# Kernel tuning notes

Hardware: AMD Instinct MI355X
Metric: run time of the kernel (lower is better)

The kernel has to match this reference:

```python
import jax, jax.numpy as jnp
import numpy as np

D_MODEL, D_FF, D_H = 1024, 4096, 64
D_H2 = D_H // 2


def layer_norm(x, w, b, eps=1e-5):
    mu = x.mean(-1, keepdims=True)
    var = x.var(-1, keepdims=True)
    return (x - mu) / jnp.sqrt(var + eps) * w + b


def gelu(x):
    return jax.nn.gelu(x, approximate=False)


def setup_inputs() -> dict:
    key = jax.random.key(0)
    ks = jax.random.split(key, 12)
    s = 0.02
    return {
        "x": jax.random.normal(ks[0], (4, 1024, D_MODEL), jnp.float32),
        "W1": jax.random.normal(ks[1], (D_FF, D_MODEL), jnp.float32) * s,
        "W2": jax.random.normal(ks[2], (D_MODEL, D_FF), jnp.float32) * s,
        "Wr1": jax.random.normal(ks[3], (D_MODEL, D_MODEL), jnp.float32) * s,
        "Wr2": jax.random.normal(ks[4], (D_FF, D_MODEL), jnp.float32) * s,
        "ln_w": jnp.ones((D_MODEL,), jnp.float32),
        "ln_b": jnp.zeros((D_MODEL,), jnp.float32),
        "phi1_w": jax.random.normal(ks[5], (D_H2, 1), jnp.float32) * s,
        "phi1_b": jnp.zeros((D_H2,), jnp.float32),
        "phi_ln1_w": jnp.ones((D_H2,), jnp.float32),
        "phi_ln1_b": jnp.zeros((D_H2,), jnp.float32),
        "phi2_w": jax.random.normal(ks[6], (D_H, D_H2), jnp.float32) * s,
        "phi2_b": jnp.zeros((D_H,), jnp.float32),
        "phi_ln2_w": jnp.ones((D_H,), jnp.float32),
        "phi_ln2_b": jnp.zeros((D_H,), jnp.float32),
        "rho1_w": jax.random.normal(ks[7], (D_H * 2, D_H), jnp.float32) * s,
        "rho1_b": jnp.zeros((D_H * 2,), jnp.float32),
        "rho2_w": jax.random.normal(ks[8], (1, D_H * 2), jnp.float32) * s,
        "rho2_b": jnp.zeros((1,), jnp.float32),
        "top_k": 256,
    }


def reference(x, W1, W2, Wr1, Wr2, ln_w, ln_b,
              phi1_w, phi1_b, phi_ln1_w, phi_ln1_b,
              phi2_w, phi2_b, phi_ln2_w, phi_ln2_b,
              rho1_w, rho1_b, rho2_w, rho2_b, top_k):
    batch, seq, d_model = x.shape
    x_flat = x.reshape(-1, d_model)                      # [T, D]
    T = x_flat.shape[0]

    # Router scores (2-layer MLP router)
    x_norm = layer_norm(x_flat, ln_w, ln_b)
    h = gelu(x_norm @ Wr1.T)
    scores = h @ Wr2.T                                   # [T, d_ff]
    top_idx = jax.lax.top_k(scores, top_k)[1]            # [T, K]

    # Dense GEMM + data-dependent top-k mask + GELU
    z = x_flat @ W1.T                                    # [T, d_ff]
    rows = jnp.arange(T)[:, None]
    mask = jnp.zeros_like(z).at[rows, top_idx].set(1.0)
    a = gelu(z * mask)

    # DeepSets manifold mixing on the selected activations
    a_sel = jnp.take_along_axis(a, top_idx, axis=-1)     # [T, K]
    e = a_sel[..., None] * phi1_w[:, 0] + phi1_b         # Linear(1 -> D_H2): [T, K, D_H2]
    e = gelu(layer_norm(e, phi_ln1_w, phi_ln1_b))
    e = layer_norm(e @ phi2_w.T + phi2_b, phi_ln2_w, phi_ln2_b)  # [T, K, D_H]
    ctx = e.mean(axis=1, keepdims=True)                  # permutation-invariant aggregate
    c = e + ctx
    r = gelu(c @ rho1_w.T + rho1_b)                      # [T, K, 2*D_H] (Dropout -> identity)
    man = (r @ rho2_w.T + rho2_b)[..., 0]                # [T, K]

    # Scatter manifold outputs back into the d_ff lane layout
    a_man = jnp.zeros_like(a).at[rows, top_idx].set(man)
    out = a_man @ W2.T                                   # [T, D]
    return out.reshape(batch, seq, d_model)
```

## Files before the change

kernel.cpp:

```cpp
#include <hip/hip_runtime.h>

#define T_TOKENS 4096
#define DM 1024
#define DF 4096
#define KSEL 256
#define DH 64
#define DH2 32
#define BAND_DELTA 1.0e-2f
#define CAP_ROW 256

typedef __attribute__((ext_vector_type(8))) short short8;
typedef __attribute__((ext_vector_type(4))) float f32x4;
typedef __attribute__((ext_vector_type(2))) float f32x2;

__device__ __forceinline__ f32x2 pkfma(f32x2 a, f32x2 b, f32x2 c) {
    return __builtin_elementwise_fma(a, b, c);
}

__device__ __forceinline__ float gelu_f(float x) {
    return 0.5f * x * (1.0f + erff(x * 0.70710678118654752440f));
}

__device__ __forceinline__ float erf_fast(float x) {
    float ax = __builtin_fabsf(x);
    float t = __builtin_amdgcn_rcpf(fmaf(0.3275911f, ax, 1.0f));
    float p = 1.061405429f;
    p = fmaf(p, t, -1.453152027f);
    p = fmaf(p, t, 1.421413741f);
    p = fmaf(p, t, -0.284496736f);
    p = fmaf(p, t, 0.254829592f);
    float e = __builtin_amdgcn_exp2f(-ax * ax * 1.44269504088896f);
    float r = fmaf(-p * t, e, 1.0f);
    return __builtin_copysignf(r, x);
}
__device__ __forceinline__ float gelu_fast(float x) {
    return 0.5f * x * (1.0f + erf_fast(x * 0.70710678118654752440f));
}

__device__ __forceinline__ unsigned short bf16_rne(float f) {
    unsigned u = __float_as_uint(f);
    unsigned r = (u + 0x7FFFu + ((u >> 16) & 1u)) >> 16;
    return (unsigned short)r;
}
__device__ __forceinline__ float bf16_to_f(unsigned short h) {
    return __uint_as_float(((unsigned)h) << 16);
}

__global__ __launch_bounds__(256) void ln_kernel(const float* __restrict__ x,
                                                 const float* __restrict__ w,
                                                 const float* __restrict__ b,
                                                 float* __restrict__ out) {
    int row = blockIdx.x;
    int tid = threadIdx.x;
    const float4 v = ((const float4*)(x + (size_t)row * DM))[tid];
    float s = v.x + v.y + v.z + v.w;
    float s2 = v.x * v.x + v.y * v.y + v.z * v.z + v.w * v.w;
#pragma unroll
    for (int off = 32; off > 0; off >>= 1) {
        s += __shfl_xor(s, off);
        s2 += __shfl_xor(s2, off);
    }
    __shared__ float ss[4], ss2[4];
    int wave = tid >> 6;
    if ((tid & 63) == 0) { ss[wave] = s; ss2[wave] = s2; }
    __syncthreads();
    s = ss[0] + ss[1] + ss[2] + ss[3];
    s2 = ss2[0] + ss2[1] + ss2[2] + ss2[3];
    float mu = s * (1.0f / DM);
    float var = s2 * (1.0f / DM) - mu * mu;
    float rs = rsqrtf(var + 1e-5f);
    const float4 wv = ((const float4*)w)[tid];
    const float4 bv = ((const float4*)b)[tid];
    float4 o;
    o.x = (v.x - mu) * rs * wv.x + bv.x;
    o.y = (v.y - mu) * rs * wv.y + bv.y;
    o.z = (v.z - mu) * rs * wv.z + bv.z;
    o.w = (v.w - mu) * rs * wv.w + bv.w;
    ((float4*)(out + (size_t)row * DM))[tid] = o;
}

__global__ __launch_bounds__(256) void gemm_f32_128(const float* __restrict__ A,
                                                    const float* __restrict__ B,
                                                    float* __restrict__ C,
                                                    int M, int N, int K, int fuse_gelu) {
    __shared__ __align__(16) float As[16][132];
    __shared__ __align__(16) float Bs[16][132];
    int tid = threadIdx.x;
    int bm = blockIdx.y * 128, bn = blockIdx.x * 128;
    int tr = tid >> 4, tc = tid & 15;

    float4 avr[2], bvr[2];
    auto g_load = [&](int k0) {
#pragma unroll
        for (int s = 0; s < 2; s++) {
            int i = tid * 2 + s;
            int r = i >> 2, q = i & 3;
            avr[s] = *(const float4*)(A + (size_t)(bm + r) * K + k0 + q * 4);
            bvr[s] = *(const float4*)(B + (size_t)(bn + r) * K + k0 + q * 4);
        }
    };

    float acc[8][8] = {};
    g_load(0);
    for (int k0 = 0; k0 < K; k0 += 16) {
        __syncthreads();
#pragma unroll
        for (int s = 0; s < 2; s++) {
            int i = tid * 2 + s;
            int r = i >> 2, q = i & 3;
            As[q * 4 + 0][r] = avr[s].x; As[q * 4 + 1][r] = avr[s].y;
            As[q * 4 + 2][r] = avr[s].z; As[q * 4 + 3][r] = avr[s].w;
            Bs[q * 4 + 0][r] = bvr[s].x; Bs[q * 4 + 1][r] = bvr[s].y;
            Bs[q * 4 + 2][r] = bvr[s].z; Bs[q * 4 + 3][r] = bvr[s].w;
        }
        __syncthreads();
        if (k0 + 16 < K) g_load(k0 + 16);
#pragma unroll
        for (int kk = 0; kk < 16; kk++) {
            float4 a0 = *(const float4*)&As[kk][tr * 4];
            float4 a1 = *(const float4*)&As[kk][64 + tr * 4];
            float4 b0 = *(const float4*)&Bs[kk][tc * 4];
            float4 b1 = *(const float4*)&Bs[kk][64 + tc * 4];
            float ar[8] = {a0.x, a0.y, a0.z, a0.w, a1.x, a1.y, a1.z, a1.w};
            float br[8] = {b0.x, b0.y, b0.z, b0.w, b1.x, b1.y, b1.z, b1.w};
#pragma unroll
            for (int i = 0; i < 8; i++)
#pragma unroll
                for (int j = 0; j < 8; j++)
                    acc[i][j] = fmaf(ar[i], br[j], acc[i][j]);
        }
    }
#pragma unroll
    for (int i = 0; i < 8; i++) {
        int row = bm + (i < 4 ? tr * 4 + i : 64 + tr * 4 + (i - 4));
        float* cp = C + (size_t)row * N + bn;
        float4 o0, o1;
        if (fuse_gelu) {
            o0 = make_float4(gelu_f(acc[i][0]), gelu_f(acc[i][1]), gelu_f(acc[i][2]), gelu_f(acc[i][3]));
            o1 = make_float4(gelu_f(acc[i][4]), gelu_f(acc[i][5]), gelu_f(acc[i][6]), gelu_f(acc[i][7]));
        } else {
            o0 = make_float4(acc[i][0], acc[i][1], acc[i][2], acc[i][3]);
            o1 = make_float4(acc[i][4], acc[i][5], acc[i][6], acc[i][7]);
        }
        *(float4*)(cp + tc * 4) = o0;
        *(float4*)(cp + 64 + tc * 4) = o1;
    }
}

__global__ __launch_bounds__(256) void gemm_bf16(const short* __restrict__ A,
                                                 const short* __restrict__ B,
                                                 float* __restrict__ C,
                                                 int M, int N, int K,
                                                 int lda, int ldb, int beta) {
    __shared__ __align__(16) short As[128 * 64];
    __shared__ __align__(16) short Bs[128 * 64];
    int tid = threadIdx.x;
    int bm = blockIdx.y * 128, bn = blockIdx.x * 128;
    int lane = tid & 63, wave = tid >> 6;
    int wm = (wave >> 1) * 64, wn = (wave & 1) * 64;
    int quad = lane >> 4, l16 = lane & 15;
    int sr = tid >> 3, scp = tid & 7;

    short8 areg[4], breg[4];
    auto g_load = [&](int k0) {
#pragma unroll
        for (int j = 0; j < 4; j++) {
            int r = j * 32 + sr;
            int cl = scp ^ (r & 7);
            areg[j] = *(const short8*)(A + (size_t)(bm + r) * lda + k0 + cl * 8);
            breg[j] = *(const short8*)(B + (size_t)(bn + r) * ldb + k0 + cl * 8);
        }
    };

    f32x4 acc[4][4] = {};
    g_load(0);
    for (int k0 = 0; k0 < K; k0 += 64) {
        __syncthreads();
#pragma unroll
        for (int j = 0; j < 4; j++) {
            *(short8*)(As + (j * 256 + tid) * 8) = areg[j];
            *(short8*)(Bs + (j * 256 + tid) * 8) = breg[j];
        }
        __syncthreads();
        if (k0 + 64 < K) g_load(k0 + 64);
#pragma unroll
        for (int kk = 0; kk < 2; kk++) {
            short8 af[4], bf[4];
#pragma unroll
            for (int tm = 0; tm < 4; tm++) {
                int m = wm + tm * 16 + l16;
                int cp = (kk * 4 + quad) ^ (m & 7);
                af[tm] = *(const short8*)(As + m * 64 + cp * 8);
            }
#pragma unroll
            for (int tn = 0; tn < 4; tn++) {
                int n = wn + tn * 16 + l16;
                int cp = (kk * 4 + quad) ^ (n & 7);
                bf[tn] = *(const short8*)(Bs + n * 64 + cp * 8);
            }
#pragma unroll
            for (int tm = 0; tm < 4; tm++)
#pragma unroll
                for (int tn = 0; tn < 4; tn++)
                    acc[tm][tn] = __builtin_amdgcn_mfma_f32_16x16x32_bf16(
                        af[tm], bf[tn], acc[tm][tn], 0, 0, 0);
        }
    }
#pragma unroll
    for (int tm = 0; tm < 4; tm++)
#pragma unroll
        for (int tn = 0; tn < 4; tn++) {
            int row0 = bm + wm + tm * 16 + quad * 4;
            int col = bn + wn + tn * 16 + l16;
#pragma unroll
            for (int r = 0; r < 4; r++) {
                float* p = C + (size_t)(row0 + r) * N + col;
                float v = acc[tm][tn][r];
                if (beta) v += *p;
                *p = v;
            }
        }
}

__global__ __launch_bounds__(256) void cvt_split_cat_kernel(const float* __restrict__ x,
                                                            short* __restrict__ cat,
                                                            int n4, int lo_first) {
    int i = blockIdx.x * 256 + threadIdx.x;
    if (i >= n4) return;
    float4 v = ((const float4*)x)[i];
    ushort4 h, l;
    h.x = bf16_rne(v.x); l.x = bf16_rne(v.x - bf16_to_f(h.x));
    h.y = bf16_rne(v.y); l.y = bf16_rne(v.y - bf16_to_f(h.y));
    h.z = bf16_rne(v.z); l.z = bf16_rne(v.z - bf16_to_f(h.z));
    h.w = bf16_rne(v.w); l.w = bf16_rne(v.w - bf16_to_f(h.w));
    int row = i >> 8;
    int col4 = i & 255;
    size_t base = (size_t)row * (2 * DM);
    size_t off_a = base + col4 * 4;
    size_t off_b = base + DM + col4 * 4;
    ((ushort4*)(cat + (lo_first ? off_b : off_a)))[0] = h;
    ((ushort4*)(cat + (lo_first ? off_a : off_b)))[0] = l;
}

__global__ __launch_bounds__(256) void cvt_bf16_kernel(const float* __restrict__ x,
                                                       short* __restrict__ y, int n4) {
    int i = blockIdx.x * 256 + threadIdx.x;
    if (i >= n4) return;
    float4 v = ((const float4*)x)[i];
    ushort4 h;
    h.x = bf16_rne(v.x); h.y = bf16_rne(v.y);
    h.z = bf16_rne(v.z); h.w = bf16_rne(v.w);
    ((ushort4*)y)[i] = h;
}

__device__ __forceinline__ unsigned sortable(float f) {
    unsigned u = __float_as_uint(f);
    return (u & 0x80000000u) ? ~u : (u | 0x80000000u);
}
__device__ __forceinline__ float unsortable(unsigned k) {
    unsigned b = (k & 0x80000000u) ? (k & 0x7FFFFFFFu) : ~k;
    return __uint_as_float(b);
}

__global__ __launch_bounds__(256) void topk_band_kernel(const float* __restrict__ scores,
                                                        int* __restrict__ cand,
                                                        int* __restrict__ cnt) {
    int row = blockIdx.x;
    int tid = threadIdx.x;
    __shared__ unsigned s_keys[DF];
    __shared__ int hist[256];
    __shared__ int sufs[256];
    __shared__ int s_misc[4];
    __shared__ int s_cnt;

    const float* sr = scores + (size_t)row * DF;
    for (int i = tid; i < DF; i += 256) s_keys[i] = sortable(sr[i]);
    if (tid == 0) s_cnt = 0;

    unsigned prefix = 0;
    int krem = KSEL;
    for (int pass = 0; pass < 4; pass++) {
        int shift = 24 - pass * 8;
        unsigned hmask = (pass == 0) ? 0u : (0xFFFFFFFFu << (shift + 8));
        hist[tid] = 0;
        __syncthreads();
        for (int i = tid; i < DF; i += 256) {
            unsigned u = s_keys[i];
            if ((u & hmask) == prefix) atomicAdd(&hist[(u >> shift) & 0xFF], 1);
        }
        __syncthreads();
        sufs[tid] = hist[tid];
        __syncthreads();
#pragma unroll
        for (int off = 1; off < 256; off <<= 1) {
            int add = (tid + off < 256) ? sufs[tid + off] : 0;
            __syncthreads();
            sufs[tid] += add;
            __syncthreads();
        }
        if (sufs[tid] >= krem && (tid == 255 || sufs[tid + 1] < krem)) {
            s_misc[0] = tid;
            s_misc[1] = sufs[tid] - hist[tid];
        }
        __syncthreads();
        prefix |= ((unsigned)s_misc[0]) << shift;
        krem -= s_misc[1];
        __syncthreads();
    }
    float vf = unsortable(prefix);
    for (int i = tid; i < DF; i += 256) {
        float d = sr[i] - vf;
        if (__builtin_fabsf(d) <= BAND_DELTA) {
            int p = atomicAdd(&s_cnt, 1);
            if (p < CAP_ROW) cand[(size_t)row * CAP_ROW + p] = i;
        }
    }
    __syncthreads();
    if (tid == 0) cnt[row] = s_cnt < CAP_ROW ? s_cnt : CAP_ROW;
}

__global__ __launch_bounds__(256) void rescore_kernel(const float* __restrict__ h,
                                                      const float* __restrict__ Wr2,
                                                      const int* __restrict__ cand,
                                                      const int* __restrict__ cnt,
                                                      float* __restrict__ scores) {
    int row = blockIdx.x;
    int lane = threadIdx.x & 63;
    int wv = threadIdx.x >> 6;
    int n = cnt[row];
    const float4* hp = (const float4*)(h + (size_t)row * DM);
    for (int c = wv; c < n; c += 4) {
        int col = cand[(size_t)row * CAP_ROW + c];
        const float4* wp = (const float4*)(Wr2 + (size_t)col * DM);
        float s = 0.f;
#pragma unroll
        for (int j = 0; j < 4; j++) {
            float4 a = hp[lane + 64 * j];
            float4 b = wp[lane + 64 * j];
            s = fmaf(a.x, b.x, s);
            s = fmaf(a.y, b.y, s);
            s = fmaf(a.z, b.z, s);
            s = fmaf(a.w, b.w, s);
        }
#pragma unroll
        for (int st = 1; st < 64; st <<= 1) s += __shfl_xor(s, st);
        if (lane == 0) scores[(size_t)row * DF + col] = s;
    }
}

__global__ __launch_bounds__(256) void topk_kernel(const float* __restrict__ scores,
                                                   int* __restrict__ top_idx) {
    int row = blockIdx.x;
    int tid = threadIdx.x;
    __shared__ unsigned s_keys[DF];
    __shared__ int hist[256];
    __shared__ int sufs[256];
    __shared__ int s_misc[4];
    __shared__ int s_wsums[4];

    const float* sr = scores + (size_t)row * DF;
    for (int i = tid; i < DF; i += 256) s_keys[i] = sortable(sr[i]);

    unsigned prefix = 0;
    int krem = KSEL;
    for (int pass = 0; pass < 4; pass++) {
        int shift = 24 - pass * 8;
        unsigned hmask = (pass == 0) ? 0u : (0xFFFFFFFFu << (shift + 8));
        hist[tid] = 0;
        __syncthreads();
        for (int i = tid; i < DF; i += 256) {
            unsigned u = s_keys[i];
            if ((u & hmask) == prefix) atomicAdd(&hist[(u >> shift) & 0xFF], 1);
        }
        __syncthreads();
        sufs[tid] = hist[tid];
        __syncthreads();
#pragma unroll
        for (int off = 1; off < 256; off <<= 1) {
            int add = (tid + off < 256) ? sufs[tid + off] : 0;
            __syncthreads();
            sufs[tid] += add;
            __syncthreads();
        }
        if (sufs[tid] >= krem && (tid == 255 || sufs[tid + 1] < krem)) {
            s_misc[0] = tid;
            s_misc[1] = sufs[tid] - hist[tid];
        }
        __syncthreads();
        prefix |= ((unsigned)s_misc[0]) << shift;
        krem -= s_misc[1];
        __syncthreads();
    }
    unsigned v = prefix;
    if (tid == 0) s_misc[2] = 0;
    __syncthreads();
    int* out = top_idx + (size_t)row * KSEL;
    for (int i = tid; i < DF; i += 256) {
        if (s_keys[i] > v) {
            int p = atomicAdd(&s_misc[2], 1);
            out[p] = i;
        }
    }
    __syncthreads();
    int base = s_misc[2];
    int lane = tid & 63, wave = tid >> 6;
    int taken = 0;
    for (int chunk = 0; chunk < DF / 256; chunk++) {
        int i = chunk * 256 + tid;
        int flag = (s_keys[i] == v) ? 1 : 0;
        unsigned long long mb = __ballot(flag);
        int before = __popcll(mb & ((1ULL << lane) - 1ULL));
        if (lane == 0) s_wsums[wave] = __popcll(mb);
        __syncthreads();
        int woff = 0;
#pragma unroll
        for (int w = 0; w < 4; w++) if (w < wave) woff += s_wsums[w];
        int total = s_wsums[0] + s_wsums[1] + s_wsums[2] + s_wsums[3];
        int excl = woff + before;
        if (flag && (taken + excl) < krem) out[base + taken + excl] = i;
        taken += total;
        __syncthreads();
    }
}

__global__ __launch_bounds__(256) void manifold_kernel(
    const float* __restrict__ z, const int* __restrict__ top_idx,
    const float* __restrict__ phi1_w, const float* __restrict__ phi1_b,
    const float* __restrict__ ln1w, const float* __restrict__ ln1b,
    const float* __restrict__ phi2_w, const float* __restrict__ phi2_b,
    const float* __restrict__ ln2w, const float* __restrict__ ln2b,
    const short* __restrict__ rho1b16, const float* __restrict__ rho1_b,
    const float* __restrict__ rho2_w, const float* __restrict__ rho2_b,
    float* __restrict__ man) {
    __shared__ __align__(16) short c_lds[256 * DH];
    __shared__ __align__(16) short w_lds[128 * DH];
    __shared__ float s_ctxp[4 * DH];
    __shared__ float s_ctx[DH];
    __shared__ float s_rho1b[2 * DH];
    __shared__ float s_rho2w[2 * DH];

    int tid = threadIdx.x;
    int t = blockIdx.x;
    int lane = tid & 63, wave = tid >> 6;
    int l16 = lane & 15, quad = lane >> 4;

    for (int b = tid; b < 128 * 8; b += 256) {
        int row = b >> 3, j = b & 7;
        *(short8*)(w_lds + row * DH + ((j ^ (row & 7)) * 8)) =
            *(const short8*)(rho1b16 + row * DH + j * 8);
    }
    if (tid < 2 * DH) { s_rho1b[tid] = rho1_b[tid]; s_rho2w[tid] = rho2_w[tid]; }

    int idx = top_idx[(size_t)t * KSEL + tid];
    float a = gelu_fast(z[(size_t)t * DF + idx]);
    f32x2 a2 = {a, a};

    f32x2 gv[DH2 / 2];
    f32x2 sv = {0.f, 0.f}, qv = {0.f, 0.f};
#pragma unroll
    for (int i = 0; i < DH2 / 2; i++) {
        f32x2 w = ((const f32x2*)phi1_w)[i];
        f32x2 b = ((const f32x2*)phi1_b)[i];
        f32x2 e = pkfma(a2, w, b);
        gv[i] = e;
        sv = sv + e;
        qv = pkfma(e, e, qv);
    }
    float s = sv.x + sv.y, s2 = qv.x + qv.y;
    float mu = s * (1.0f / DH2);
    float rs = rsqrtf(s2 * (1.0f / DH2) - mu * mu + 1e-5f);
    f32x2 muv = {mu, mu}, rsv = {rs, rs};
#pragma unroll
    for (int i = 0; i < DH2 / 2; i++) {
        f32x2 t2 = (gv[i] - muv) * rsv;
        t2 = pkfma(t2, ((const f32x2*)ln1w)[i], ((const f32x2*)ln1b)[i]);
        gv[i] = (f32x2){gelu_fast(t2.x), gelu_fast(t2.y)};
    }

    f32x2 hv[DH / 2];
#pragma unroll
    for (int j2 = 0; j2 < DH / 2; j2++) {
        const f32x2* wa = (const f32x2*)(phi2_w + (2 * j2) * DH2);
        const f32x2* wb = (const f32x2*)(phi2_w + (2 * j2 + 1) * DH2);
        f32x2 ra = {phi2_b[2 * j2], 0.f};
        f32x2 rb = {phi2_b[2 * j2 + 1], 0.f};
#pragma unroll
        for (int i = 0; i < DH2 / 2; i++) {
            ra = pkfma(gv[i], wa[i], ra);
            rb = pkfma(gv[i], wb[i], rb);
        }
        hv[j2] = (f32x2){ra.x + ra.y, rb.x + rb.y};
    }

    f32x2 tsv = {0.f, 0.f}, tqv = {0.f, 0.f};
#pragma unroll
    for (int j2 = 0; j2 < DH / 2; j2++) {
        tsv = tsv + hv[j2];
        tqv = pkfma(hv[j2], hv[j2], tqv);
    }
    float tsum = tsv.x + tsv.y, tsq = tqv.x + tqv.y;
    float mu2 = tsum * (1.0f / DH);
    float rs2 = rsqrtf(tsq * (1.0f / DH) - mu2 * mu2 + 1e-5f);
    f32x2 mu2v = {mu2, mu2}, rs2v = {rs2, rs2};
#pragma unroll
    for (int j2 = 0; j2 < DH / 2; j2++) {
        f32x2 t2 = (hv[j2] - mu2v) * rs2v;
        hv[j2] = pkfma(t2, ((const f32x2*)ln2w)[j2], ((const f32x2*)ln2b)[j2]);
    }

#pragma unroll
    for (int j2 = 0; j2 < DH / 2; j2++) {
        float vx = hv[j2].x, vy = hv[j2].y;
#pragma unroll
        for (int st = 1; st < 64; st <<= 1) {
            vx += __shfl_xor(vx, st);
            vy += __shfl_xor(vy, st);
        }
        if (lane == 0) {
            s_ctxp[wave * DH + 2 * j2] = vx;
            s_ctxp[wave * DH + 2 * j2 + 1] = vy;
        }
    }
    __syncthreads();
    if (tid < DH)
        s_ctx[tid] = (s_ctxp[tid] + s_ctxp[DH + tid] + s_ctxp[2 * DH + tid] +
                      s_ctxp[3 * DH + tid]) * (1.0f / KSEL);
    __syncthreads();

#pragma unroll
    for (int j = 0; j < 8; j++) {
        short8 pk;
#pragma unroll
        for (int i2 = 0; i2 < 4; i2++) {
            f32x2 v = hv[4 * j + i2] + ((const f32x2*)s_ctx)[4 * j + i2];
            pk[2 * i2] = (short)bf16_rne(v.x);
            pk[2 * i2 + 1] = (short)bf16_rne(v.y);
        }
        *(short8*)(c_lds + tid * DH + ((j ^ (tid & 7)) * 8)) = pk;
    }
    __syncthreads();

    int wbase = wave * 64;
    short8 af[4][2];
#pragma unroll
    for (int tm = 0; tm < 4; tm++)
#pragma unroll
        for (int kf = 0; kf < 2; kf++) {
            int m = wbase + tm * 16 + l16;
            int cl = (kf * 4 + quad) ^ (m & 7);
            af[tm][kf] = *(const short8*)(c_lds + m * DH + cl * 8);
        }
    float mpart[4][4] = {};
#pragma unroll
    for (int tn = 0; tn < 8; tn++) {
        int n = tn * 16 + l16;
        short8 bf[2];
#pragma unroll
        for (int kf = 0; kf < 2; kf++) {
            int cl = (kf * 4 + quad) ^ (n & 7);
            bf[kf] = *(const short8*)(w_lds + n * DH + cl * 8);
        }
        f32x4 acc[4] = {};
#pragma unroll
        for (int kf = 0; kf < 2; kf++)
#pragma unroll
            for (int tm = 0; tm < 4; tm++)
                acc[tm] = __builtin_amdgcn_mfma_f32_16x16x32_bf16(
                    af[tm][kf], bf[kf], acc[tm], 0, 0, 0);
        float b1 = s_rho1b[n];
        float w2v = s_rho2w[n];
#pragma unroll
        for (int tm = 0; tm < 4; tm++)
#pragma unroll
            for (int r = 0; r < 4; r++)
                mpart[tm][r] = fmaf(gelu_fast(acc[tm][r] + b1), w2v, mpart[tm][r]);
    }
#pragma unroll
    for (int tm = 0; tm < 4; tm++)
#pragma unroll
        for (int r = 0; r < 4; r++) {
            float v = mpart[tm][r];
            v += __shfl_xor(v, 1);
            v += __shfl_xor(v, 2);
            v += __shfl_xor(v, 4);
            v += __shfl_xor(v, 8);
            mpart[tm][r] = v;
        }
    if (l16 == 0) {
        float b2 = rho2_b[0];
#pragma unroll
        for (int tm = 0; tm < 4; tm++)
#pragma unroll
            for (int r = 0; r < 4; r++)
                man[(size_t)t * KSEL + wbase + tm * 16 + quad * 4 + r] =
                    mpart[tm][r] + b2;
    }
}

__global__ __launch_bounds__(256) void scatter_bf16_kernel(const float* __restrict__ man,
                                                           const int* __restrict__ top_idx,
                                                           short* __restrict__ a_man) {
    int t = blockIdx.x, k = threadIdx.x;
    a_man[(size_t)t * DF + top_idx[(size_t)t * KSEL + k]] =
        (short)bf16_rne(man[(size_t)t * KSEL + k]);
}

extern "C" void kernel_launch(void* const* d_in, const int* in_sizes, int n_in,
                              void* d_out, int out_size, void* d_ws, size_t ws_size,
                              hipStream_t stream) {
    const float* x      = (const float*)d_in[0];
    const float* W1     = (const float*)d_in[1];
    const float* W2     = (const float*)d_in[2];
    const float* Wr1    = (const float*)d_in[3];
    const float* Wr2    = (const float*)d_in[4];
    const float* ln_w   = (const float*)d_in[5];
    const float* ln_b   = (const float*)d_in[6];
    const float* phi1_w = (const float*)d_in[7];
    const float* phi1_b = (const float*)d_in[8];
    const float* pl1w   = (const float*)d_in[9];
    const float* pl1b   = (const float*)d_in[10];
    const float* phi2_w = (const float*)d_in[11];
    const float* phi2_b = (const float*)d_in[12];
    const float* pl2w   = (const float*)d_in[13];
    const float* pl2b   = (const float*)d_in[14];
    const float* rho1_w = (const float*)d_in[15];
    const float* rho1_b = (const float*)d_in[16];
    const float* rho2_w = (const float*)d_in[17];
    const float* rho2_b = (const float*)d_in[18];
    float* out = (float*)d_out;

    char* ws = (char*)d_ws;
    size_t off = 0;
    auto alloc = [&](size_t bytes) {
        char* p = ws + off;
        off += (bytes + 255) & ~(size_t)255;
        return p;
    };
    float* xn     = (float*)alloc(sizeof(float) * (size_t)T_TOKENS * DM);
    float* h      = (float*)alloc(sizeof(float) * (size_t)T_TOKENS * DM);
    float* scores = (float*)alloc(sizeof(float) * (size_t)T_TOKENS * DF);
    float* z      = (float*)alloc(sizeof(float) * (size_t)T_TOKENS * DF);
    int*   tidx   = (int*)alloc(sizeof(int) * (size_t)T_TOKENS * KSEL);
    float* man    = (float*)alloc(sizeof(float) * (size_t)T_TOKENS * KSEL);
    int*   cand   = (int*)alloc(sizeof(int) * (size_t)T_TOKENS * CAP_ROW);
    int*   cnt    = (int*)alloc(sizeof(int) * (size_t)T_TOKENS);
    short* rho1b16 = (short*)alloc(sizeof(short) * 2 * DH * DH);

    short* h_hi   = (short*)z;
    short* wr2_hi = (short*)z + (size_t)T_TOKENS * DM;
    short* xcat  = (short*)xn;
    short* w1cat = (short*)h;
    short* amanb = (short*)scores;
    short* w2b   = (short*)z;

    ln_kernel<<<T_TOKENS, 256, 0, stream>>>(x, ln_w, ln_b, xn);
    gemm_f32_128<<<dim3(DM / 128, T_TOKENS / 128), 256, 0, stream>>>(xn, Wr1, h, T_TOKENS, DM, DM, 1);
    cvt_bf16_kernel<<<(T_TOKENS * DM / 4 + 255) / 256, 256, 0, stream>>>(h, h_hi, T_TOKENS * DM / 4);
    cvt_bf16_kernel<<<(DF * DM / 4 + 255) / 256, 256, 0, stream>>>(Wr2, wr2_hi, DF * DM / 4);
    gemm_bf16<<<dim3(DF / 128, T_TOKENS / 128), 256, 0, stream>>>(
        h_hi, wr2_hi, scores, T_TOKENS, DF, DM, DM, DM, 0);
    topk_band_kernel<<<T_TOKENS, 256, 0, stream>>>(scores, cand, cnt);
    rescore_kernel<<<T_TOKENS, 256, 0, stream>>>(h, Wr2, cand, cnt, scores);
    topk_kernel<<<T_TOKENS, 256, 0, stream>>>(scores, tidx);
    cvt_split_cat_kernel<<<(T_TOKENS * DM / 4 + 255) / 256, 256, 0, stream>>>(x, xcat, T_TOKENS * DM / 4, 0);
    cvt_split_cat_kernel<<<(DF * DM / 4 + 255) / 256, 256, 0, stream>>>(W1, w1cat, DF * DM / 4, 1);
    cvt_bf16_kernel<<<(2 * DH * DH / 4 + 255) / 256, 256, 0, stream>>>(rho1_w, rho1b16, 2 * DH * DH / 4);
    gemm_bf16<<<dim3(DF / 128, T_TOKENS / 128), 256, 0, stream>>>(
        xcat, w1cat + DM, z, T_TOKENS, DF, DM, 2 * DM, 2 * DM, 0);
    gemm_bf16<<<dim3(DF / 128, T_TOKENS / 128), 256, 0, stream>>>(
        xcat, w1cat, z, T_TOKENS, DF, 2 * DM, 2 * DM, 2 * DM, 1);
    manifold_kernel<<<T_TOKENS, 256, 0, stream>>>(z, tidx, phi1_w, phi1_b, pl1w, pl1b,
                                                  phi2_w, phi2_b, pl2w, pl2b,
                                                  rho1b16, rho1_b, rho2_w, rho2_b, man);
    hipMemsetAsync(amanb, 0, sizeof(short) * (size_t)T_TOKENS * DF, stream);
    scatter_bf16_kernel<<<T_TOKENS, 256, 0, stream>>>(man, tidx, amanb);
    cvt_bf16_kernel<<<(DM * DF / 4 + 255) / 256, 256, 0, stream>>>(W2, w2b, DM * DF / 4);
    gemm_bf16<<<dim3(DM / 128, T_TOKENS / 128), 256, 0, stream>>>(
        amanb, w2b, out, T_TOKENS, DM, DF, DF, DF, 0);
}
```

Baseline: 929.4 us.

## Use single fp16 GEMM for W1/W2 and replace full top-k with band-only selection

Replaces the split hi/lo bf16 W1 GEMM (two passes, effective K of 2048 plus 1024) with a single fp16 GEMM on a new f16 MFMA kernel, and switches the W2 GEMM to fp16 as well. The top-k path no longer rescans all 4096 scores a second time. The band kernel writes confidently-above indices directly, and a small rank-based selection over the rescored band candidates fills the remaining slots. This cuts GEMM work and one full radix pass per row, at the cost of fp16 range and precision risk for the z values that feed top-k activations.

```diff
diff --git a/kernel.cpp b/kernel.cpp
--- a/kernel.cpp
+++ b/kernel.cpp
@@ -10,6 +10,7 @@
 #define CAP_ROW 256
 
 typedef __attribute__((ext_vector_type(8))) short short8;
+typedef __attribute__((ext_vector_type(8))) _Float16 half8;
 typedef __attribute__((ext_vector_type(4))) float f32x4;
 typedef __attribute__((ext_vector_type(2))) float f32x2;
 
@@ -41,9 +42,6 @@
     unsigned u = __float_as_uint(f);
     unsigned r = (u + 0x7FFFu + ((u >> 16) & 1u)) >> 16;
     return (unsigned short)r;
-}
-__device__ __forceinline__ float bf16_to_f(unsigned short h) {
-    return __uint_as_float(((unsigned)h) << 16);
 }
 
 __global__ __launch_bounds__(256) void ln_kernel(const float* __restrict__ x,
@@ -222,24 +220,76 @@
         }
 }
 
-__global__ __launch_bounds__(256) void cvt_split_cat_kernel(const float* __restrict__ x,
-                                                            short* __restrict__ cat,
-                                                            int n4, int lo_first) {
-    int i = blockIdx.x * 256 + threadIdx.x;
-    if (i >= n4) return;
-    float4 v = ((const float4*)x)[i];
-    ushort4 h, l;
-    h.x = bf16_rne(v.x); l.x = bf16_rne(v.x - bf16_to_f(h.x));
-    h.y = bf16_rne(v.y); l.y = bf16_rne(v.y - bf16_to_f(h.y));
-    h.z = bf16_rne(v.z); l.z = bf16_rne(v.z - bf16_to_f(h.z));
-    h.w = bf16_rne(v.w); l.w = bf16_rne(v.w - bf16_to_f(h.w));
-    int row = i >> 8;
-    int col4 = i & 255;
-    size_t base = (size_t)row * (2 * DM);
-    size_t off_a = base + col4 * 4;
-    size_t off_b = base + DM + col4 * 4;
-    ((ushort4*)(cat + (lo_first ? off_b : off_a)))[0] = h;
-    ((ushort4*)(cat + (lo_first ? off_a : off_b)))[0] = l;
+__global__ __launch_bounds__(256) void gemm_f16(const short* __restrict__ A,
+                                                const short* __restrict__ B,
+                                                float* __restrict__ C,
+                                                int M, int N, int K,
+                                                int lda, int ldb) {
+    __shared__ __align__(16) short As[128 * 64];
+    __shared__ __align__(16) short Bs[128 * 64];
+    int tid = threadIdx.x;
+    int bm = blockIdx.y * 128, bn = blockIdx.x * 128;
+    int lane = tid & 63, wave = tid >> 6;
+    int wm = (wave >> 1) * 64, wn = (wave & 1) * 64;
+    int quad = lane >> 4, l16 = lane & 15;
+    int sr = tid >> 3, scp = tid & 7;
+
+    short8 areg[4], breg[4];
+    auto g_load = [&](int k0) {
+#pragma unroll
+        for (int j = 0; j < 4; j++) {
+            int r = j * 32 + sr;
+            int cl = scp ^ (r & 7);
+            areg[j] = *(const short8*)(A + (size_t)(bm + r) * lda + k0 + cl * 8);
+            breg[j] = *(const short8*)(B + (size_t)(bn + r) * ldb + k0 + cl * 8);
+        }
+    };
+
+    f32x4 acc[4][4] = {};
+    g_load(0);
+    for (int k0 = 0; k0 < K; k0 += 64) {
+        __syncthreads();
+#pragma unroll
+        for (int j = 0; j < 4; j++) {
+            *(short8*)(As + (j * 256 + tid) * 8) = areg[j];
+            *(short8*)(Bs + (j * 256 + tid) * 8) = breg[j];
+        }
+        __syncthreads();
+        if (k0 + 64 < K) g_load(k0 + 64);
+#pragma unroll
+        for (int kk = 0; kk < 2; kk++) {
+            short8 af[4], bf[4];
+#pragma unroll
+            for (int tm = 0; tm < 4; tm++) {
+                int m = wm + tm * 16 + l16;
+                int cp = (kk * 4 + quad) ^ (m & 7);
+                af[tm] = *(const short8*)(As + m * 64 + cp * 8);
+            }
+#pragma unroll
+            for (int tn = 0; tn < 4; tn++) {
+                int n = wn + tn * 16 + l16;
+                int cp = (kk * 4 + quad) ^ (n & 7);
+                bf[tn] = *(const short8*)(Bs + n * 64 + cp * 8);
+            }
+#pragma unroll
+            for (int tm = 0; tm < 4; tm++)
+#pragma unroll
+                for (int tn = 0; tn < 4; tn++)
+                    acc[tm][tn] = __builtin_amdgcn_mfma_f32_16x16x32_f16(
+                        __builtin_bit_cast(half8, af[tm]),
+                        __builtin_bit_cast(half8, bf[tn]), acc[tm][tn], 0, 0, 0);
+        }
+    }
+#pragma unroll
+    for (int tm = 0; tm < 4; tm++)
+#pragma unroll
+        for (int tn = 0; tn < 4; tn++) {
+            int row0 = bm + wm + tm * 16 + quad * 4;
+            int col = bn + wn + tn * 16 + l16;
+#pragma unroll
+            for (int r = 0; r < 4; r++)
+                C[(size_t)(row0 + r) * N + col] = acc[tm][tn][r];
+        }
 }
 
 __global__ __launch_bounds__(256) void cvt_bf16_kernel(const float* __restrict__ x,
@@ -253,6 +303,19 @@
     ((ushort4*)y)[i] = h;
 }
 
+__global__ __launch_bounds__(256) void cvt_f16_kernel(const float* __restrict__ x,
+                                                      short* __restrict__ y, int n4) {
+    int i = blockIdx.x * 256 + threadIdx.x;
+    if (i >= n4) return;
+    float4 v = ((const float4*)x)[i];
+    ushort4 h;
+    h.x = __builtin_bit_cast(unsigned short, (_Float16)v.x);
+    h.y = __builtin_bit_cast(unsigned short, (_Float16)v.y);
+    h.z = __builtin_bit_cast(unsigned short, (_Float16)v.z);
+    h.w = __builtin_bit_cast(unsigned short, (_Float16)v.w);
+    ((ushort4*)y)[i] = h;
+}
+
 __device__ __forceinline__ unsigned sortable(float f) {
     unsigned u = __float_as_uint(f);
     return (u & 0x80000000u) ? ~u : (u | 0x80000000u);
@@ -263,19 +326,21 @@
 }
 
 __global__ __launch_bounds__(256) void topk_band_kernel(const float* __restrict__ scores,
+                                                        int* __restrict__ tidx,
                                                         int* __restrict__ cand,
-                                                        int* __restrict__ cnt) {
+                                                        int* __restrict__ cnt,
+                                                        int* __restrict__ na_arr) {
     int row = blockIdx.x;
     int tid = threadIdx.x;
     __shared__ unsigned s_keys[DF];
     __shared__ int hist[256];
     __shared__ int sufs[256];
     __shared__ int s_misc[4];
-    __shared__ int s_cnt;
+    __shared__ int s_cnt, s_na;
 
     const float* sr = scores + (size_t)row * DF;
     for (int i = tid; i < DF; i += 256) s_keys[i] = sortable(sr[i]);
-    if (tid == 0) s_cnt = 0;
+    if (tid == 0) { s_cnt = 0; s_na = 0; }
 
     unsigned prefix = 0;
     int krem = KSEL;
@@ -308,22 +373,29 @@
         __syncthreads();
     }
     float vf = unsortable(prefix);
+    int* out = tidx + (size_t)row * KSEL;
     for (int i = tid; i < DF; i += 256) {
         float d = sr[i] - vf;
-        if (__builtin_fabsf(d) <= BAND_DELTA) {
+        if (d > BAND_DELTA) {
+            int p = atomicAdd(&s_na, 1);
+            out[p] = i;
+        } else if (d >= -BAND_DELTA) {
             int p = atomicAdd(&s_cnt, 1);
             if (p < CAP_ROW) cand[(size_t)row * CAP_ROW + p] = i;
         }
     }
     __syncthreads();
-    if (tid == 0) cnt[row] = s_cnt < CAP_ROW ? s_cnt : CAP_ROW;
+    if (tid == 0) {
+        cnt[row] = s_cnt < CAP_ROW ? s_cnt : CAP_ROW;
+        na_arr[row] = s_na;
+    }
 }
 
 __global__ __launch_bounds__(256) void rescore_kernel(const float* __restrict__ h,
                                                       const float* __restrict__ Wr2,
                                                       const int* __restrict__ cand,
                                                       const int* __restrict__ cnt,
-                                                      float* __restrict__ scores) {
+                                                      float* __restrict__ bscore) {
     int row = blockIdx.x;
     int lane = threadIdx.x & 63;
     int wv = threadIdx.x >> 6;
@@ -344,82 +416,37 @@
         }
 #pragma unroll
         for (int st = 1; st < 64; st <<= 1) s += __shfl_xor(s, st);
-        if (lane == 0) scores[(size_t)row * DF + col] = s;
-    }
-}
-
-__global__ __launch_bounds__(256) void topk_kernel(const float* __restrict__ scores,
-                                                   int* __restrict__ top_idx) {
+        if (lane == 0) bscore[(size_t)row * CAP_ROW + c] = s;
+    }
+}
+
+__global__ __launch_bounds__(256) void band_select_kernel(const float* __restrict__ bscore,
+                                                          const int* __restrict__ cand,
+                                                          const int* __restrict__ cnt,
+                                                          const int* __restrict__ na_arr,
+                                                          int* __restrict__ tidx) {
     int row = blockIdx.x;
     int tid = threadIdx.x;
-    __shared__ unsigned s_keys[DF];
-    __shared__ int hist[256];
-    __shared__ int sufs[256];
-    __shared__ int s_misc[4];
-    __shared__ int s_wsums[4];
-
-    const float* sr = scores + (size_t)row * DF;
-    for (int i = tid; i < DF; i += 256) s_keys[i] = sortable(sr[i]);
-
-    unsigned prefix = 0;
-    int krem = KSEL;
-    for (int pass = 0; pass < 4; pass++) {
-        int shift = 24 - pass * 8;
-        unsigned hmask = (pass == 0) ? 0u : (0xFFFFFFFFu << (shift + 8));
-        hist[tid] = 0;
-        __syncthreads();
-        for (int i = tid; i < DF; i += 256) {
-            unsigned u = s_keys[i];
-            if ((u & hmask) == prefix) atomicAdd(&hist[(u >> shift) & 0xFF], 1);
-        }
-        __syncthreads();
-        sufs[tid] = hist[tid];
-        __syncthreads();
-#pragma unroll
-        for (int off = 1; off < 256; off <<= 1) {
-            int add = (tid + off < 256) ? sufs[tid + off] : 0;
-            __syncthreads();
-            sufs[tid] += add;
-            __syncthreads();
-        }
-        if (sufs[tid] >= krem && (tid == 255 || sufs[tid + 1] < krem)) {
-            s_misc[0] = tid;
-            s_misc[1] = sufs[tid] - hist[tid];
-        }
-        __syncthreads();
-        prefix |= ((unsigned)s_misc[0]) << shift;
-        krem -= s_misc[1];
-        __syncthreads();
-    }
-    unsigned v = prefix;
-    if (tid == 0) s_misc[2] = 0;
+    int n = cnt[row];
+    int na = na_arr[row];
+    int m = KSEL - na;
+    __shared__ float ss[CAP_ROW];
+    __shared__ int si[CAP_ROW];
+    for (int i = tid; i < n; i += 256) {
+        ss[i] = bscore[(size_t)row * CAP_ROW + i];
+        si[i] = cand[(size_t)row * CAP_ROW + i];
+    }
     __syncthreads();
-    int* out = top_idx + (size_t)row * KSEL;
-    for (int i = tid; i < DF; i += 256) {
-        if (s_keys[i] > v) {
-            int p = atomicAdd(&s_misc[2], 1);
-            out[p] = i;
-        }
-    }
-    __syncthreads();
-    int base = s_misc[2];
-    int lane = tid & 63, wave = tid >> 6;
-    int taken = 0;
-    for (int chunk = 0; chunk < DF / 256; chunk++) {
-        int i = chunk * 256 + tid;
-        int flag = (s_keys[i] == v) ? 1 : 0;
-        unsigned long long mb = __ballot(flag);
-        int before = __popcll(mb & ((1ULL << lane) - 1ULL));
-        if (lane == 0) s_wsums[wave] = __popcll(mb);
-        __syncthreads();
-        int woff = 0;
-#pragma unroll
-        for (int w = 0; w < 4; w++) if (w < wave) woff += s_wsums[w];
-        int total = s_wsums[0] + s_wsums[1] + s_wsums[2] + s_wsums[3];
-        int excl = woff + before;
-        if (flag && (taken + excl) < krem) out[base + taken + excl] = i;
-        taken += total;
-        __syncthreads();
+    if (tid < n) {
+        float s = ss[tid];
+        int idx = si[tid];
+        int rank = 0;
+        for (int j = 0; j < n; j++) {
+            float sj = ss[j];
+            int ij = si[j];
+            rank += (sj > s) || (sj == s && ij < idx);
+        }
+        if (rank < m) tidx[(size_t)row * KSEL + na + rank] = idx;
     }
 }
 
@@ -597,12 +624,12 @@
     }
 }
 
-__global__ __launch_bounds__(256) void scatter_bf16_kernel(const float* __restrict__ man,
-                                                           const int* __restrict__ top_idx,
-                                                           short* __restrict__ a_man) {
+__global__ __launch_bounds__(256) void scatter_f16_kernel(const float* __restrict__ man,
+                                                          const int* __restrict__ top_idx,
+                                                          short* __restrict__ a_man) {
     int t = blockIdx.x, k = threadIdx.x;
     a_man[(size_t)t * DF + top_idx[(size_t)t * KSEL + k]] =
-        (short)bf16_rne(man[(size_t)t * KSEL + k]);
+        __builtin_bit_cast(short, (_Float16)man[(size_t)t * KSEL + k]);
 }
 
 extern "C" void kernel_launch(void* const* d_in, const int* in_sizes, int n_in,
@@ -643,15 +670,17 @@
     int*   tidx   = (int*)alloc(sizeof(int) * (size_t)T_TOKENS * KSEL);
     float* man    = (float*)alloc(sizeof(float) * (size_t)T_TOKENS * KSEL);
     int*   cand   = (int*)alloc(sizeof(int) * (size_t)T_TOKENS * CAP_ROW);
+    float* bscore = (float*)alloc(sizeof(float) * (size_t)T_TOKENS * CAP_ROW);
     int*   cnt    = (int*)alloc(sizeof(int) * (size_t)T_TOKENS);
+    int*   na_arr = (int*)alloc(sizeof(int) * (size_t)T_TOKENS);
     short* rho1b16 = (short*)alloc(sizeof(short) * 2 * DH * DH);
 
     short* h_hi   = (short*)z;
     short* wr2_hi = (short*)z + (size_t)T_TOKENS * DM;
-    short* xcat  = (short*)xn;
-    short* w1cat = (short*)h;
-    short* amanb = (short*)scores;
-    short* w2b   = (short*)z;
+    short* xf16   = (short*)xn;
+    short* w1f16  = (short*)h;
+    short* amanb  = (short*)scores;
+    short* w2f16  = (short*)z;
 
     ln_kernel<<<T_TOKENS, 256, 0, stream>>>(x, ln_w, ln_b, xn);
     gemm_f32_128<<<dim3(DM / 128, T_TOKENS / 128), 256, 0, stream>>>(xn, Wr1, h, T_TOKENS, DM, DM, 1);
@@ -659,22 +688,20 @@
     cvt_bf16_kernel<<<(DF * DM / 4 + 255) / 256, 256, 0, stream>>>(Wr2, wr2_hi, DF * DM / 4);
     gemm_bf16<<<dim3(DF / 128, T_TOKENS / 128), 256, 0, stream>>>(
         h_hi, wr2_hi, scores, T_TOKENS, DF, DM, DM, DM, 0);
-    topk_band_kernel<<<T_TOKENS, 256, 0, stream>>>(scores, cand, cnt);
-    rescore_kernel<<<T_TOKENS, 256, 0, stream>>>(h, Wr2, cand, cnt, scores);
-    topk_kernel<<<T_TOKENS, 256, 0, stream>>>(scores, tidx);
-    cvt_split_cat_kernel<<<(T_TOKENS * DM / 4 + 255) / 256, 256, 0, stream>>>(x, xcat, T_TOKENS * DM / 4, 0);
-    cvt_split_cat_kernel<<<(DF * DM / 4 + 255) / 256, 256, 0, stream>>>(W1, w1cat, DF * DM / 4, 1);
+    topk_band_kernel<<<T_TOKENS, 256, 0, stream>>>(scores, tidx, cand, cnt, na_arr);
+    rescore_kernel<<<T_TOKENS, 256, 0, stream>>>(h, Wr2, cand, cnt, bscore);
+    band_select_kernel<<<T_TOKENS, 256, 0, stream>>>(bscore, cand, cnt, na_arr, tidx);
+    cvt_f16_kernel<<<(T_TOKENS * DM / 4 + 255) / 256, 256, 0, stream>>>(x, xf16, T_TOKENS * DM / 4);
+    cvt_f16_kernel<<<(DF * DM / 4 + 255) / 256, 256, 0, stream>>>(W1, w1f16, DF * DM / 4);
     cvt_bf16_kernel<<<(2 * DH * DH / 4 + 255) / 256, 256, 0, stream>>>(rho1_w, rho1b16, 2 * DH * DH / 4);
-    gemm_bf16<<<dim3(DF / 128, T_TOKENS / 128), 256, 0, stream>>>(
-        xcat, w1cat + DM, z, T_TOKENS, DF, DM, 2 * DM, 2 * DM, 0);
-    gemm_bf16<<<dim3(DF / 128, T_TOKENS / 128), 256, 0, stream>>>(
-        xcat, w1cat, z, T_TOKENS, DF, 2 * DM, 2 * DM, 2 * DM, 1);
+    gemm_f16<<<dim3(DF / 128, T_TOKENS / 128), 256, 0, stream>>>(
+        xf16, w1f16, z, T_TOKENS, DF, DM, DM, DM);
     manifold_kernel<<<T_TOKENS, 256, 0, stream>>>(z, tidx, phi1_w, phi1_b, pl1w, pl1b,
                                                   phi2_w, phi2_b, pl2w, pl2b,
                                                   rho1b16, rho1_b, rho2_w, rho2_b, man);
     hipMemsetAsync(amanb, 0, sizeof(short) * (size_t)T_TOKENS * DF, stream);
-    scatter_bf16_kernel<<<T_TOKENS, 256, 0, stream>>>(man, tidx, amanb);
-    cvt_bf16_kernel<<<(DM * DF / 4 + 255) / 256, 256, 0, stream>>>(W2, w2b, DM * DF / 4);
-    gemm_bf16<<<dim3(DM / 128, T_TOKENS / 128), 256, 0, stream>>>(
-        amanb, w2b, out, T_TOKENS, DM, DF, DF, DF, 0);
-}
+    scatter_f16_kernel<<<T_TOKENS, 256, 0, stream>>>(man, tidx, amanb);
+    cvt_f16_kernel<<<(DM * DF / 4 + 255) / 256, 256, 0, stream>>>(W2, w2f16, DM * DF / 4);
+    gemm_f16<<<dim3(DM / 128, T_TOKENS / 128), 256, 0, stream>>>(
+        amanb, w2f16, out, T_TOKENS, DM, DF, DF, DF);
+}
```

Result: faster. 776.0 us (-16.5%).
